# Performance work log

Measured on AMD Instinct MI355X. Metric: run time of the kernel, lower is better.

## Reference

```python
import jax, jax.numpy as jnp
import numpy as np

K = 3
PAD = 1


def bilinear_gather(xr, py, px):
    # xr: [B, G, H, W, C] channels-last per offset group; py/px: [B, G, H, W] sample coords
    B, G, H, W, C = xr.shape
    y0 = jnp.floor(py)
    x0 = jnp.floor(px)
    wy = py - y0
    wx = px - x0
    y0i = y0.astype(jnp.int32)
    x0i = x0.astype(jnp.int32)
    bi = jnp.arange(B)[:, None, None, None]
    gi = jnp.arange(G)[None, :, None, None]
    out = jnp.zeros(py.shape + (C,), xr.dtype)
    corners = (
        (0, 0, (1 - wy) * (1 - wx)),
        (0, 1, (1 - wy) * wx),
        (1, 0, wy * (1 - wx)),
        (1, 1, wy * wx),
    )
    for dy_, dx_, w in corners:
        yy = y0i + dy_
        xx = x0i + dx_
        valid = ((yy >= 0) & (yy < H) & (xx >= 0) & (xx < W)).astype(xr.dtype)
        yc = jnp.clip(yy, 0, H - 1)
        xc = jnp.clip(xx, 0, W - 1)
        v = xr[bi, gi, yc, xc]  # [B,G,H,W,C]
        out = out + (w * valid)[..., None] * v
    return out


def setup_inputs() -> dict:
    key = jax.random.key(0)
    k1, k2, k3, k4, k5 = jax.random.split(key, 5)
    B, Cin, H, W = 4, 64, 256, 256
    G, OC = 8, 64
    KK = K * K
    x = jax.random.normal(k1, (B, Cin, H, W), jnp.float32)
    offset = jax.random.normal(k2, (B, 2, G * KK, H, W), jnp.float32)
    mask = jax.random.normal(k3, (B, G * KK, H, W), jnp.float32)
    weight = jax.random.normal(k4, (OC, Cin // G, K, K), jnp.float32) * 0.05
    bias = jax.random.normal(k5, (OC,), jnp.float32) * 0.01
    return {"x": x, "offset": offset, "mask": mask, "weight": weight, "bias": bias}


def reference(x, offset, mask, weight, bias):
    B, Cin, H, W = x.shape
    OC, Cpg, _, _ = weight.shape
    G = Cin // Cpg          # conv groups == offset groups here
    OPG = OC // G
    KK = K * K
    # replicate module's permute(0,2,1,3,4).flip(1).view(b,-1,fh,fw):
    # pair axis (dy,dx) is input dim 1; combined (group,tap) axis is reversed
    off = jnp.flip(offset, axis=2)                      # [B,2,G*KK,H,W]
    dy = off[:, 0].reshape(B, G, KK, H, W)
    dx = off[:, 1].reshape(B, G, KK, H, W)
    m = jax.nn.sigmoid(mask).reshape(B, G, KK, H, W)
    xr = x.reshape(B, G, Cpg, H, W).transpose(0, 1, 3, 4, 2)  # [B,G,H,W,Cpg]
    wg = weight.reshape(G, OPG, Cpg, K, K)
    iy = jnp.arange(H, dtype=x.dtype)[None, None, :, None]
    ix = jnp.arange(W, dtype=x.dtype)[None, None, None, :]
    out = jnp.zeros((B, G, OPG, H, W), x.dtype)
    for t in range(KK):  # fixed small loop over kernel taps
        ki, kj = t // K, t % K
        py = iy - PAD + ki + dy[:, :, t]
        px = ix - PAD + kj + dx[:, :, t]
        s = bilinear_gather(xr, py, px) * m[:, :, t][..., None]  # [B,G,H,W,Cpg]
        out = out + jnp.einsum('bghwc,gdc->bgdhw', s, wg[:, :, :, ki, kj])
    return out.reshape(B, OC, H, W) + bias[None, :, None, None]
```

## Files before the change

kernel.cpp:

```cpp
#include <hip/hip_runtime.h>
#include <hip/hip_fp16.h>


#define KSZ 3
#define PAD 1

static constexpr int B   = 4;
static constexpr int Cin = 64;
static constexpr int H   = 256;
static constexpr int W   = 256;
static constexpr int G   = 8;
static constexpr int OC  = 64;
static constexpr int KK  = KSZ * KSZ;
static constexpr int Cpg = Cin / G;
static constexpr int OPG = OC / G;
static constexpr int HW  = H * W;
static constexpr int NXCD = 8;

static constexpr int BR    = 4;
static constexpr int BC    = 64;
static constexpr int MARG  = 5;
static constexpr int WROWS = BR + 2 * MARG + 1;
static constexpr int WCOLS = 75;
static constexpr int WUSED = BC + 2 * MARG;

typedef _Float16 f16x8  __attribute__((ext_vector_type(8)));
typedef float    f32x16 __attribute__((ext_vector_type(16)));

union U4H {
    uint4 u;
    __half2 h2[4];
    _Float16 h[8];
    f16x8 v;
};

__global__ __launch_bounds__(256) void transpose_kernel(
    const float* __restrict__ x, uint4* __restrict__ xt)
{
    const int h = blockIdx.x, g = blockIdx.y, b = blockIdx.z;
    const int w = threadIdx.x;
    const int pix = h * W + w;
    const float* src = x + (size_t)(b * Cin + g * Cpg) * HW + pix;
    U4H v;
#pragma unroll
    for (int c = 0; c < 8; ++c) v.h[c] = (_Float16)src[(size_t)c * HW];
    xt[(size_t)(b * G + g) * HW + pix] = v.u;
}

__global__ __launch_bounds__(320) void prep_weights(
    const float* __restrict__ weight, uint4* __restrict__ wfrag)
{
    const int g    = blockIdx.x;
    const int tid  = threadIdx.x;
    const int m    = tid >> 6;
    const int lane = tid & 63;
    const int hi   = lane >> 5;
    const int lp   = lane & 31;
    const int t    = 2 * m + hi;
    U4H a;
#pragma unroll
    for (int c = 0; c < 8; ++c) {
        float v = 0.0f;
        if (lp < OPG && t < KK)
            v = weight[((size_t)(g * OPG + lp) * Cpg + c) * KK + t];
        a.h[c] = (_Float16)v;
    }
    wfrag[((size_t)g * 5 + m) * 64 + lane] = a.u;
}

__device__ __attribute__((noinline)) f16x8 slow_sample(
    const uint4* __restrict__ xb, int y0, int x0, float wy, float wx, float ms)
{
    const bool vy0 = (unsigned)y0 < (unsigned)H;
    const bool vy1 = (unsigned)(y0 + 1) < (unsigned)H;
    const bool vx0 = (unsigned)x0 < (unsigned)W;
    const bool vx1 = (unsigned)(x0 + 1) < (unsigned)W;
    const float u  = vy0 ? (1.f - wy) * ms : 0.f;
    const float vv = vy1 ? wy * ms : 0.f;
    const float ca = vx0 ? (1.f - wx) : 0.f;
    const float cb = vx1 ? wx : 0.f;
    const float w00 = u * ca, w01 = u * cb, w10 = vv * ca, w11 = vv * cb;
    const int yc0 = min(max(y0, 0), H - 1), yc1 = min(max(y0 + 1, 0), H - 1);
    const int xc0 = min(max(x0, 0), W - 1), xc1 = min(max(x0 + 1, 0), W - 1);
    U4H a, bq, c, d;
    a.u  = xb[yc0 * W + xc0];
    bq.u = xb[yc0 * W + xc1];
    c.u  = xb[yc1 * W + xc0];
    d.u  = xb[yc1 * W + xc1];
    const __half2 h00 = __float2half2_rn(w00);
    const __half2 h01 = __float2half2_rn(w01);
    const __half2 h10 = __float2half2_rn(w10);
    const __half2 h11 = __float2half2_rn(w11);
    U4H s;
#pragma unroll
    for (int i = 0; i < 4; ++i)
        s.h2[i] = __hfma2(h00, a.h2[i],
                  __hfma2(h01, bq.h2[i],
                  __hfma2(h10, c.h2[i],
                  __hmul2(h11, d.h2[i]))));
    return s.v;
}

__global__ __launch_bounds__(256) void dcn_kernel(
    const uint4* __restrict__ xt,
    const uint4* __restrict__ wfrag,
    const float* __restrict__ offset,
    const float* __restrict__ mask,
    const float* __restrict__ bias,
    float* __restrict__ out)
{
    __shared__ uint4 win[WROWS * WCOLS];

    const unsigned id = blockIdx.x;
    const unsigned wl = (id & (NXCD - 1)) * (gridDim.x / NXCD) + (id >> 3);
    const int colblk = wl & 3;
    const int rowblk = (wl >> 2) & 63;
    const int g      = (wl >> 8) & (G - 1);
    const int b      = wl >> 11;

    const int h_base = rowblk * BR;
    const int xbase  = colblk * BC;
    const int h0     = h_base - MARG;
    const int x0base = xbase - MARG;

    const int tid  = threadIdx.x;
    const int lane = tid & 63;
    const int wave = tid >> 6;
    const int hi   = lane >> 5;
    const int lp   = lane & 31;

    const int h = h_base + wave;

    const uint4* xb = xt + (size_t)(b * G + g) * HW;

#pragma unroll
    for (int it = 0; it < 5; ++it) {
        const int k = it * 256 + tid;
        if (k < WROWS * WCOLS) {
            const int i = k / WCOLS;
            const int j = k - i * WCOLS;
            const int gr = h0 + i;
            const int gc = x0base + j;
            const bool vld = ((unsigned)gr < (unsigned)H) & ((unsigned)gc < (unsigned)W);
            const int grc = min(max(gr, 0), H - 1);
            const int gcc = min(max(gc, 0), W - 1);
            uint4 val = xb[grc * W + gcc];
            if (!vld) val = make_uint4(0, 0, 0, 0);
            win[k] = val;
        }
    }

    const float* offy = offset + (size_t)(b * 2 + 0) * (G * KK) * HW;
    const float* offx = offset + (size_t)(b * 2 + 1) * (G * KK) * HW;
    const float* mk   = mask + (size_t)b * (G * KK) * HW;
    const uint4* wfb  = wfrag + (size_t)g * 5 * 64 + lane;

    const int pix0 = h * W + xbase + lp;
    const int pix1 = pix0 + 32;

    float dy0c, dx0c, mv0c, dy1c, dx1c, mv1c;
    U4H afc;
    {
        const int t0  = hi;
        const int oI = (G * KK - 1 - (g * KK + t0)) * HW;
        const int mI = (g * KK + t0) * HW;
        dy0c = offy[oI + pix0];  dx0c = offx[oI + pix0];  mv0c = mk[mI + pix0];
        dy1c = offy[oI + pix1];  dx1c = offx[oI + pix1];  mv1c = mk[mI + pix1];
        afc.u = wfb[0];
    }

    __syncthreads();

    auto sample = [&](float py, float px, float ms) -> f16x8 {
        const float y0f = floorf(py), x0f = floorf(px);
        const float wy = py - y0f, wx = px - x0f;
        const int y0 = (int)y0f, x0 = (int)x0f;
        const int iy0 = y0 - h0;
        const int ix0 = x0 - x0base;
        const bool ok = ((unsigned)iy0 <= (unsigned)(WROWS - 2)) &
                        ((unsigned)ix0 <= (unsigned)(WUSED - 2));
        int a0 = iy0 * WCOLS + ix0;
        a0 = ok ? a0 : 0;
        U4H a, bq, c, d;
        a.u  = win[a0];          bq.u = win[a0 + 1];
        c.u  = win[a0 + WCOLS];  d.u  = win[a0 + WCOLS + 1];
        const float u  = (1.f - wy) * ms;
        const float vv = wy * ms;
        const float w00 = u * (1.f - wx), w01 = u * wx;
        const float w10 = vv * (1.f - wx), w11 = vv * wx;
        const __half2 h00 = __float2half2_rn(w00);
        const __half2 h01 = __float2half2_rn(w01);
        const __half2 h10 = __float2half2_rn(w10);
        const __half2 h11 = __float2half2_rn(w11);
        U4H s;
#pragma unroll
        for (int i = 0; i < 4; ++i)
            s.h2[i] = __hfma2(h00, a.h2[i],
                      __hfma2(h01, bq.h2[i],
                      __hfma2(h10, c.h2[i],
                      __hmul2(h11, d.h2[i]))));
        f16x8 res = s.v;
        if (__builtin_expect(!__all((int)ok), 0)) {
            if (!ok) res = slow_sample(xb, y0, x0, wy, wx, ms);
        }
        return res;
    };

    f32x16 acc0 = {};
    f32x16 acc1 = {};

#pragma unroll 1
    for (int m = 0; m < 5; ++m) {
        const int mn  = (m < 4) ? m + 1 : 4;
        const int tn  = 2 * mn + hi;
        const int ttn = (tn > 8) ? 8 : tn;
        const int oIn = (G * KK - 1 - (g * KK + ttn)) * HW;
        const int mIn = (g * KK + ttn) * HW;
        const float dy0n = offy[oIn + pix0];
        const float dx0n = offx[oIn + pix0];
        const float mv0n = mk[mIn + pix0];
        const float dy1n = offy[oIn + pix1];
        const float dx1n = offx[oIn + pix1];
        const float mv1n = mk[mIn + pix1];
        U4H afn; afn.u = wfb[mn * 64];

        const int t  = 2 * m + hi;
        const int tt = (t > 8) ? 8 : t;
        const int ki = (tt >= 3) + (tt >= 6);
        const int kj = tt - 3 * ki;
        const float pyb = (float)(h - PAD + ki);
        const float pxb = (float)(xbase + lp - PAD + kj);

        float sg0 = 1.0f / (1.0f + __expf(-mv0c));
        float sg1 = 1.0f / (1.0f + __expf(-mv1c));
        sg0 = (t <= 8) ? sg0 : 0.0f;
        sg1 = (t <= 8) ? sg1 : 0.0f;

        acc0 = __builtin_amdgcn_mfma_f32_32x32x16_f16(
            afc.v, sample(pyb + dy0c, pxb + dx0c, sg0), acc0, 0, 0, 0);
        acc1 = __builtin_amdgcn_mfma_f32_32x32x16_f16(
            afc.v, sample(pyb + dy1c, pxb + 32.0f + dx1c, sg1), acc1, 0, 0, 0);

        dy0c = dy0n; dx0c = dx0n; mv0c = mv0n;
        dy1c = dy1n; dx1c = dx1n; mv1c = mv1n;
        afc = afn;
    }

#pragma unroll
    for (int tile = 0; tile < 2; ++tile) {
        const int wq = xbase + tile * 32 + lp;
#pragma unroll
        for (int r = 0; r < 4; ++r) {
            const int dd = r + 4 * hi;
            const float v = (tile == 0 ? acc0[r] : acc1[r]) + bias[g * OPG + dd];
            out[((size_t)b * OC + g * OPG + dd) * HW + h * W + wq] = v;
        }
    }
}

extern "C" void kernel_launch(void* const* d_in, const int* in_sizes, int n_in,
                              void* d_out, int out_size, void* d_ws, size_t ws_size,
                              hipStream_t stream) {
    const float* x      = (const float*)d_in[0];
    const float* offset = (const float*)d_in[1];
    const float* mask   = (const float*)d_in[2];
    const float* weight = (const float*)d_in[3];
    const float* bias   = (const float*)d_in[4];
    float* out = (float*)d_out;

    uint4* xt    = (uint4*)d_ws;
    uint4* wfrag = (uint4*)((char*)d_ws + (size_t)B * G * HW * 16);

    dim3 tgrid(H, G, B);
    transpose_kernel<<<tgrid, dim3(256), 0, stream>>>(x, xt);
    prep_weights<<<dim3(G), dim3(320), 0, stream>>>(weight, wfrag);
    dcn_kernel<<<dim3(B * G * (H / BR) * (W / BC)), dim3(256), 0, stream>>>(
        xt, wfrag, offset, mask, bias, out);
}
```

Before: 99.40 us.

## Widen DCN block tile to 128 columns with four MFMA accumulators per wave

Doubles the column tile handled per block from 64 to 128 pixels, so each wave now processes four 32-pixel sub-tiles with four accumulators. The shared-memory halo window grows to 139 columns, which shrinks the relative halo overhead and halves the number of blocks. The cost is twice the LDS per block (about 33 KB), more registers per thread for the prefetched offsets and accumulators, and lower occupancy and block count, which may hurt latency hiding.

```diff
diff --git a/kernel.cpp b/kernel.cpp
--- a/kernel.cpp
+++ b/kernel.cpp
@@ -18,11 +18,12 @@
 static constexpr int NXCD = 8;
 
 static constexpr int BR    = 4;
-static constexpr int BC    = 64;
+static constexpr int BC    = 128;
 static constexpr int MARG  = 5;
 static constexpr int WROWS = BR + 2 * MARG + 1;
-static constexpr int WCOLS = 75;
+static constexpr int WCOLS = 139;
 static constexpr int WUSED = BC + 2 * MARG;
+static constexpr int WSLOTS = WROWS * WCOLS;
 
 typedef _Float16 f16x8  __attribute__((ext_vector_type(8)));
 typedef float    f32x16 __attribute__((ext_vector_type(16)));
@@ -109,14 +110,14 @@
     const float* __restrict__ bias,
     float* __restrict__ out)
 {
-    __shared__ uint4 win[WROWS * WCOLS];
+    __shared__ uint4 win[WSLOTS];
 
     const unsigned id = blockIdx.x;
     const unsigned wl = (id & (NXCD - 1)) * (gridDim.x / NXCD) + (id >> 3);
-    const int colblk = wl & 3;
-    const int rowblk = (wl >> 2) & 63;
-    const int g      = (wl >> 8) & (G - 1);
-    const int b      = wl >> 11;
+    const int colblk = wl & 1;
+    const int rowblk = (wl >> 1) & 63;
+    const int g      = (wl >> 7) & (G - 1);
+    const int b      = wl >> 10;
 
     const int h_base = rowblk * BR;
     const int xbase  = colblk * BC;
@@ -134,9 +135,9 @@
     const uint4* xb = xt + (size_t)(b * G + g) * HW;
 
 #pragma unroll
-    for (int it = 0; it < 5; ++it) {
+    for (int it = 0; it < 9; ++it) {
         const int k = it * 256 + tid;
-        if (k < WROWS * WCOLS) {
+        if (k < WSLOTS) {
             const int i = k / WCOLS;
             const int j = k - i * WCOLS;
             const int gr = h0 + i;
@@ -156,16 +157,19 @@
     const uint4* wfb  = wfrag + (size_t)g * 5 * 64 + lane;
 
     const int pix0 = h * W + xbase + lp;
-    const int pix1 = pix0 + 32;
-
-    float dy0c, dx0c, mv0c, dy1c, dx1c, mv1c;
+
+    float dyc[4], dxc[4], mvc[4];
     U4H afc;
     {
-        const int t0  = hi;
+        const int t0 = hi;
         const int oI = (G * KK - 1 - (g * KK + t0)) * HW;
         const int mI = (g * KK + t0) * HW;
-        dy0c = offy[oI + pix0];  dx0c = offx[oI + pix0];  mv0c = mk[mI + pix0];
-        dy1c = offy[oI + pix1];  dx1c = offx[oI + pix1];  mv1c = mk[mI + pix1];
+#pragma unroll
+        for (int q = 0; q < 4; ++q) {
+            dyc[q] = offy[oI + pix0 + 32 * q];
+            dxc[q] = offx[oI + pix0 + 32 * q];
+            mvc[q] = mk[mI + pix0 + 32 * q];
+        }
         afc.u = wfb[0];
     }
 
@@ -206,8 +210,7 @@
         return res;
     };
 
-    f32x16 acc0 = {};
-    f32x16 acc1 = {};
+    f32x16 acc0 = {}, acc1 = {}, acc2 = {}, acc3 = {};
 
 #pragma unroll 1
     for (int m = 0; m < 5; ++m) {
@@ -216,12 +219,13 @@
         const int ttn = (tn > 8) ? 8 : tn;
         const int oIn = (G * KK - 1 - (g * KK + ttn)) * HW;
         const int mIn = (g * KK + ttn) * HW;
-        const float dy0n = offy[oIn + pix0];
-        const float dx0n = offx[oIn + pix0];
-        const float mv0n = mk[mIn + pix0];
-        const float dy1n = offy[oIn + pix1];
-        const float dx1n = offx[oIn + pix1];
-        const float mv1n = mk[mIn + pix1];
+        float dyn[4], dxn[4], mvn[4];
+#pragma unroll
+        for (int q = 0; q < 4; ++q) {
+            dyn[q] = offy[oIn + pix0 + 32 * q];
+            dxn[q] = offx[oIn + pix0 + 32 * q];
+            mvn[q] = mk[mIn + pix0 + 32 * q];
+        }
         U4H afn; afn.u = wfb[mn * 64];
 
         const int t  = 2 * m + hi;
@@ -231,30 +235,38 @@
         const float pyb = (float)(h - PAD + ki);
         const float pxb = (float)(xbase + lp - PAD + kj);
 
-        float sg0 = 1.0f / (1.0f + __expf(-mv0c));
-        float sg1 = 1.0f / (1.0f + __expf(-mv1c));
-        sg0 = (t <= 8) ? sg0 : 0.0f;
-        sg1 = (t <= 8) ? sg1 : 0.0f;
+        float sg[4];
+#pragma unroll
+        for (int q = 0; q < 4; ++q) {
+            float s = 1.0f / (1.0f + __expf(-mvc[q]));
+            sg[q] = (t <= 8) ? s : 0.0f;
+        }
 
         acc0 = __builtin_amdgcn_mfma_f32_32x32x16_f16(
-            afc.v, sample(pyb + dy0c, pxb + dx0c, sg0), acc0, 0, 0, 0);
+            afc.v, sample(pyb + dyc[0], pxb + dxc[0], sg[0]), acc0, 0, 0, 0);
         acc1 = __builtin_amdgcn_mfma_f32_32x32x16_f16(
-            afc.v, sample(pyb + dy1c, pxb + 32.0f + dx1c, sg1), acc1, 0, 0, 0);
-
-        dy0c = dy0n; dx0c = dx0n; mv0c = mv0n;
-        dy1c = dy1n; dx1c = dx1n; mv1c = mv1n;
+            afc.v, sample(pyb + dyc[1], pxb + 32.0f + dxc[1], sg[1]), acc1, 0, 0, 0);
+        acc2 = __builtin_amdgcn_mfma_f32_32x32x16_f16(
+            afc.v, sample(pyb + dyc[2], pxb + 64.0f + dxc[2], sg[2]), acc2, 0, 0, 0);
+        acc3 = __builtin_amdgcn_mfma_f32_32x32x16_f16(
+            afc.v, sample(pyb + dyc[3], pxb + 96.0f + dxc[3], sg[3]), acc3, 0, 0, 0);
+
+#pragma unroll
+        for (int q = 0; q < 4; ++q) {
+            dyc[q] = dyn[q]; dxc[q] = dxn[q]; mvc[q] = mvn[q];
+        }
         afc = afn;
     }
 
 #pragma unroll
-    for (int tile = 0; tile < 2; ++tile) {
-        const int wq = xbase + tile * 32 + lp;
-#pragma unroll
-        for (int r = 0; r < 4; ++r) {
-            const int dd = r + 4 * hi;
-            const float v = (tile == 0 ? acc0[r] : acc1[r]) + bias[g * OPG + dd];
-            out[((size_t)b * OC + g * OPG + dd) * HW + h * W + wq] = v;
-        }
+    for (int r = 0; r < 4; ++r) {
+        const int dd = r + 4 * hi;
+        float* ob = out + ((size_t)b * OC + g * OPG + dd) * HW + h * W + xbase + lp;
+        const float bv = bias[g * OPG + dd];
+        ob[0]  = acc0[r] + bv;
+        ob[32] = acc1[r] + bv;
+        ob[64] = acc2[r] + bv;
+        ob[96] = acc3[r] + bv;
     }
 }
 
```

Measured after the change: 96.66 us. 2.8% less time.

## Fuse NCHW-to-channels-last fp16 transpose into the DCN window load

Applied to the files above, without the earlier changes.

Removes the separate transpose kernel and its fp16 channels-last workspace. The DCN kernel now reads the 8 channels of each pixel straight from the fp32 NCHW input while filling the shared-memory window, and converts them to fp16 there. The slow out-of-window sampling path also reads fp32 planes directly. This saves a kernel launch and a full write-then-read of the transposed tensor, but each window slot now needs 8 strided 4-byte loads instead of one 16-byte load, and neighbouring blocks re-read overlapping halo rows.

```diff
diff --git a/kernel.cpp b/kernel.cpp
--- a/kernel.cpp
+++ b/kernel.cpp
@@ -23,6 +23,7 @@
 static constexpr int WROWS = BR + 2 * MARG + 1;
 static constexpr int WCOLS = 75;
 static constexpr int WUSED = BC + 2 * MARG;
+static constexpr int WSLOTS = WROWS * WCOLS;
 
 typedef _Float16 f16x8  __attribute__((ext_vector_type(8)));
 typedef float    f32x16 __attribute__((ext_vector_type(16)));
@@ -33,19 +34,6 @@
     _Float16 h[8];
     f16x8 v;
 };
-
-__global__ __launch_bounds__(256) void transpose_kernel(
-    const float* __restrict__ x, uint4* __restrict__ xt)
-{
-    const int h = blockIdx.x, g = blockIdx.y, b = blockIdx.z;
-    const int w = threadIdx.x;
-    const int pix = h * W + w;
-    const float* src = x + (size_t)(b * Cin + g * Cpg) * HW + pix;
-    U4H v;
-#pragma unroll
-    for (int c = 0; c < 8; ++c) v.h[c] = (_Float16)src[(size_t)c * HW];
-    xt[(size_t)(b * G + g) * HW + pix] = v.u;
-}
 
 __global__ __launch_bounds__(320) void prep_weights(
     const float* __restrict__ weight, uint4* __restrict__ wfrag)
@@ -69,7 +57,7 @@
 }
 
 __device__ __attribute__((noinline)) f16x8 slow_sample(
-    const uint4* __restrict__ xb, int y0, int x0, float wy, float wx, float ms)
+    const float* __restrict__ xsrc, int y0, int x0, float wy, float wx, float ms)
 {
     const bool vy0 = (unsigned)y0 < (unsigned)H;
     const bool vy1 = (unsigned)(y0 + 1) < (unsigned)H;
@@ -82,34 +70,26 @@
     const float w00 = u * ca, w01 = u * cb, w10 = vv * ca, w11 = vv * cb;
     const int yc0 = min(max(y0, 0), H - 1), yc1 = min(max(y0 + 1, 0), H - 1);
     const int xc0 = min(max(x0, 0), W - 1), xc1 = min(max(x0 + 1, 0), W - 1);
-    U4H a, bq, c, d;
-    a.u  = xb[yc0 * W + xc0];
-    bq.u = xb[yc0 * W + xc1];
-    c.u  = xb[yc1 * W + xc0];
-    d.u  = xb[yc1 * W + xc1];
-    const __half2 h00 = __float2half2_rn(w00);
-    const __half2 h01 = __float2half2_rn(w01);
-    const __half2 h10 = __float2half2_rn(w10);
-    const __half2 h11 = __float2half2_rn(w11);
+    const int o00 = yc0 * W + xc0, o01 = yc0 * W + xc1;
+    const int o10 = yc1 * W + xc0, o11 = yc1 * W + xc1;
     U4H s;
 #pragma unroll
-    for (int i = 0; i < 4; ++i)
-        s.h2[i] = __hfma2(h00, a.h2[i],
-                  __hfma2(h01, bq.h2[i],
-                  __hfma2(h10, c.h2[i],
-                  __hmul2(h11, d.h2[i]))));
+    for (int c = 0; c < 8; ++c) {
+        const float* p = xsrc + (size_t)c * HW;
+        s.h[c] = (_Float16)(w00 * p[o00] + w01 * p[o01] + w10 * p[o10] + w11 * p[o11]);
+    }
     return s.v;
 }
 
 __global__ __launch_bounds__(256) void dcn_kernel(
-    const uint4* __restrict__ xt,
+    const float* __restrict__ x,
     const uint4* __restrict__ wfrag,
     const float* __restrict__ offset,
     const float* __restrict__ mask,
     const float* __restrict__ bias,
     float* __restrict__ out)
 {
-    __shared__ uint4 win[WROWS * WCOLS];
+    __shared__ uint4 win[WSLOTS];
 
     const unsigned id = blockIdx.x;
     const unsigned wl = (id & (NXCD - 1)) * (gridDim.x / NXCD) + (id >> 3);
@@ -131,22 +111,24 @@
 
     const int h = h_base + wave;
 
-    const uint4* xb = xt + (size_t)(b * G + g) * HW;
+    const float* xsrc = x + (size_t)(b * Cin + g * Cpg) * HW;
 
 #pragma unroll
     for (int it = 0; it < 5; ++it) {
         const int k = it * 256 + tid;
-        if (k < WROWS * WCOLS) {
+        if (k < WSLOTS) {
             const int i = k / WCOLS;
             const int j = k - i * WCOLS;
             const int gr = h0 + i;
             const int gc = x0base + j;
             const bool vld = ((unsigned)gr < (unsigned)H) & ((unsigned)gc < (unsigned)W);
-            const int grc = min(max(gr, 0), H - 1);
-            const int gcc = min(max(gc, 0), W - 1);
-            uint4 val = xb[grc * W + gcc];
-            if (!vld) val = make_uint4(0, 0, 0, 0);
-            win[k] = val;
+            const int addr = min(max(gr, 0), H - 1) * W + min(max(gc, 0), W - 1);
+            U4H v;
+#pragma unroll
+            for (int c = 0; c < 8; ++c)
+                v.h[c] = (_Float16)xsrc[addr + (size_t)c * HW];
+            if (!vld) v.u = make_uint4(0, 0, 0, 0);
+            win[k] = v.u;
         }
     }
 
@@ -201,7 +183,7 @@
                       __hmul2(h11, d.h2[i]))));
         f16x8 res = s.v;
         if (__builtin_expect(!__all((int)ok), 0)) {
-            if (!ok) res = slow_sample(xb, y0, x0, wy, wx, ms);
+            if (!ok) res = slow_sample(xsrc, y0, x0, wy, wx, ms);
         }
         return res;
     };
@@ -268,12 +250,9 @@
     const float* bias   = (const float*)d_in[4];
     float* out = (float*)d_out;
 
-    uint4* xt    = (uint4*)d_ws;
-    uint4* wfrag = (uint4*)((char*)d_ws + (size_t)B * G * HW * 16);
-
-    dim3 tgrid(H, G, B);
-    transpose_kernel<<<tgrid, dim3(256), 0, stream>>>(x, xt);
+    uint4* wfrag = (uint4*)d_ws;
+
     prep_weights<<<dim3(G), dim3(320), 0, stream>>>(weight, wfrag);
     dcn_kernel<<<dim3(B * G * (H / BR) * (W / BC)), dim3(256), 0, stream>>>(
-        xt, wfrag, offset, mask, bias, out);
-}
+        x, wfrag, offset, mask, bias, out);
+}
```

New measurement: 103.8 us. +4.4%, slower.
